# Kernel tuning notes

Hardware: AMD Instinct MI355X
Metric: run time of the kernel (lower is better)

## Reference

```python
import jax, jax.numpy as jnp
import numpy as np

N_HEADS = 16


def setup_inputs() -> dict:
    key = jax.random.key(0)
    ks = jax.random.split(key, 7)
    B, S, E = 4, 2048, 1024
    s = 0.02
    return {
        "x": jax.random.normal(ks[0], (B, S, E), dtype=jnp.float32),
        "Wq": jax.random.normal(ks[1], (E, E), dtype=jnp.float32) * s,
        "bq": jax.random.normal(ks[2], (E,), dtype=jnp.float32) * s,
        "Wk": jax.random.normal(ks[3], (E, E), dtype=jnp.float32) * s,
        "bk": jax.random.normal(ks[4], (E,), dtype=jnp.float32) * s,
        "Wv": jax.random.normal(ks[5], (E, E), dtype=jnp.float32) * s,
        "bv": jax.random.normal(ks[6], (E,), dtype=jnp.float32) * s,
    }


def reference(x, Wq, bq, Wk, bk, Wv, bv):
    B, S, E = x.shape
    H = N_HEADS
    D = E // H  # att_dim
    scale = 1.0 / jnp.sqrt(jnp.asarray(D, dtype=x.dtype))
    # torch Linear: y = x @ W.T + b
    q = (x @ Wq.T + bq).reshape(B, S, H, D)
    k = (x @ Wk.T + bk).reshape(B, S, H, D)
    v = (x @ Wv.T + bv).reshape(B, S, H, D)
    # scores: [B, H, S, S]
    scores = jnp.einsum("bqhd,bkhd->bhqk", q, k) * scale
    attn = jax.nn.softmax(scores, axis=-1)
    out = jnp.einsum("bhqk,bkhd->bqhd", attn, v)
    return out.reshape(B, S, E)
```

## Files before the change

kernel.cpp:

```cpp
#include <hip/hip_runtime.h>
#include <stdint.h>
#include <math.h>

typedef __bf16 bf16;
typedef __attribute__((ext_vector_type(8))) __bf16 bf16x8;
typedef __attribute__((ext_vector_type(4))) __bf16 bf16x4;
typedef __attribute__((ext_vector_type(4))) float f32x4;
typedef unsigned short u16;
typedef unsigned int u32;

#define BATCH 4
#define SEQ   2048
#define EMB   1024
#define HEADS 16
#define HDIM  64
#define BH    (BATCH*HEADS)

#define QSCALE 0.125f

#define OFF_XB 0u
#define OFF_WC 16777216u
#define OFF_Q  23068672u
#define OFF_K  39845888u
#define OFF_VT 56623104u

#define DRAIN_VM asm volatile("s_waitcnt vmcnt(0)" ::: "memory")
#define FENCE_LDS do { \
    asm volatile("s_waitcnt lgkmcnt(0)" ::: "memory"); \
    __builtin_amdgcn_sched_barrier(0); \
} while (0)


__device__ __forceinline__ u16 f2bf(float f) {
    u32 b = __builtin_bit_cast(u32, f);
    return (u16)((b + 0x7fffu + ((b >> 16) & 1u)) >> 16);
}

__global__ void cvt_all(const float* __restrict__ x,
                        const float* __restrict__ wq, const float* __restrict__ wk,
                        const float* __restrict__ wv,
                        u16* __restrict__ xb, u16* __restrict__ wc) {
    const int X4 = (BATCH * SEQ * EMB) / 4;
    const int W4 = (EMB * EMB) / 4;
    const int n4 = X4 + 3 * W4;
    int stride = gridDim.x * blockDim.x;
    for (int i = blockIdx.x * blockDim.x + threadIdx.x; i < n4; i += stride) {
        const float* src; u16* dst; int j;
        if (i < X4)              { src = x;  dst = xb;                j = i; }
        else if (i < X4 + W4)    { src = wq; dst = wc;                j = i - X4; }
        else if (i < X4 + 2*W4)  { src = wk; dst = wc + EMB * EMB;    j = i - X4 - W4; }
        else                     { src = wv; dst = wc + 2 * EMB * EMB; j = i - X4 - 2 * W4; }
        float4 v = reinterpret_cast<const float4*>(src)[j];
        ushort4 o;
        o.x = f2bf(v.x); o.y = f2bf(v.y); o.z = f2bf(v.z); o.w = f2bf(v.w);
        reinterpret_cast<ushort4*>(dst)[j] = o;
    }
}

__global__ __launch_bounds__(256, 3) void qkv_gemm(
    const u16* __restrict__ xb, const u16* __restrict__ wc,
    const float* __restrict__ bq, const float* __restrict__ bk_, const float* __restrict__ bv,
    u16* __restrict__ Qw, u16* __restrict__ Kw, u16* __restrict__ Vt)
{
    __shared__ u16 lds[2 * 128 * 64];
    const int tid = threadIdx.x;
    const int w = tid >> 6, l = tid & 63;
    const int hi = l >> 4, lo = l & 15;
    const int bm = blockIdx.x & 63;
    const int bn = blockIdx.x >> 6;
    const int wm = w >> 1, wn = w & 1;

    const int srow   = l >> 3;
    const int schunk = (l & 7) ^ (srow & 7);

    f32x4 acc[4][4];
#pragma unroll
    for (int i = 0; i < 4; ++i)
#pragma unroll
        for (int j = 0; j < 4; ++j) acc[i][j] = f32x4{0.f, 0.f, 0.f, 0.f};

    for (int t = 0; t < 16; ++t) {
        const u16* asrc = xb + (size_t)(bm * 128 + srow) * 1024 + t * 64 + schunk * 8;
        const u16* bsrc = wc + (size_t)(bn * 128 + srow) * 1024 + t * 64 + schunk * 8;
#pragma unroll
        for (int i = 0; i < 4; ++i) {
            int c = i * 4 + w;
            __builtin_amdgcn_global_load_lds(
                (const __attribute__((address_space(1))) u32*)(asrc + (size_t)c * 8 * 1024),
                (__attribute__((address_space(3))) u32*)(&lds[c * 512]), 16, 0, 0);
            __builtin_amdgcn_global_load_lds(
                (const __attribute__((address_space(1))) u32*)(bsrc + (size_t)c * 8 * 1024),
                (__attribute__((address_space(3))) u32*)(&lds[128 * 64 + c * 512]), 16, 0, 0);
        }
        DRAIN_VM;
        __syncthreads();
#pragma unroll
        for (int kk = 0; kk < 2; ++kk) {
            bf16x8 af[4], bfr[4];
#pragma unroll
            for (int mt = 0; mt < 4; ++mt) {
                int row = wm * 64 + mt * 16 + lo;
                int off = (kk * 64 + hi * 16) ^ ((row & 7) << 4);
                af[mt] = *reinterpret_cast<const bf16x8*>((const char*)lds + row * 128 + off);
            }
#pragma unroll
            for (int nt = 0; nt < 4; ++nt) {
                int row = wn * 64 + nt * 16 + lo;
                int off = (kk * 64 + hi * 16) ^ ((row & 7) << 4);
                bfr[nt] = *reinterpret_cast<const bf16x8*>((const char*)lds + 128 * 64 * 2 + row * 128 + off);
            }
#pragma unroll
            for (int mt = 0; mt < 4; ++mt)
#pragma unroll
                for (int nt = 0; nt < 4; ++nt)
                    acc[mt][nt] = __builtin_amdgcn_mfma_f32_16x16x32_bf16(af[mt], bfr[nt], acc[mt][nt], 0, 0, 0);
        }
        __syncthreads();
    }

#pragma unroll
    for (int nt = 0; nt < 4; ++nt) {
        int ng  = bn * 128 + wn * 64 + nt * 16 + lo;
        int mat = ng >> 10;
        int nl  = ng & 1023;
        int h = nl >> 6, d = nl & 63;
        const float* bp = (mat == 0) ? bq : (mat == 1 ? bk_ : bv);
        float bias = bp[nl];
        float scl = (mat == 0) ? QSCALE : 1.0f;
#pragma unroll
        for (int mt = 0; mt < 4; ++mt) {
            int mbase = bm * 128 + wm * 64 + mt * 16 + hi * 4;
            int b = mbase >> 11, s = mbase & 2047;
            if (mat < 2) {
                u16* dst = (mat == 0) ? Qw : Kw;
                size_t base = ((size_t)(b * 16 + h) * 2048) * 64 + (size_t)d;
#pragma unroll
                for (int r = 0; r < 4; ++r)
                    dst[base + (size_t)(s + r) * 64] = f2bf((acc[mt][nt][r] + bias) * scl);
            } else {
                ushort4 o;
                o.x = f2bf(acc[mt][nt][0] + bias);
                o.y = f2bf(acc[mt][nt][1] + bias);
                o.z = f2bf(acc[mt][nt][2] + bias);
                o.w = f2bf(acc[mt][nt][3] + bias);
                *reinterpret_cast<ushort4*>(&Vt[((size_t)(b * 16 + h) * 64 + d) * 2048 + s]) = o;
            }
        }
    }
}

#define KVB 64
__global__ __launch_bounds__(512, 4) void attn(
    const u16* __restrict__ Qw, const u16* __restrict__ Kw, const u16* __restrict__ Vt,
    float* __restrict__ out)
{
    __shared__ char smem[69632];
    const int tid = threadIdx.x;
    const int w = tid >> 6, l = tid & 63;
    const int hi = l >> 4, lo = l & 15;

    const int bid = blockIdx.x;
    const int xcd = bid & 7, ii = bid >> 3;
    const int bh = xcd * 8 + (ii & 7);
    const int qt = ii >> 3;
    const int bb = bh >> 4, h = bh & 15;
    const int q0w = qt * 256 + w * 32;

    const u16* Qb = Qw + ((size_t)bh * 2048 + q0w) * 64;
    const u16* Kb = Kw + (size_t)bh * 2048 * 64;
    const u16* Vb = Vt + (size_t)bh * 64 * 2048;
    char* bufs = smem;
    char* myP  = smem + 32768 + w * 4608;

    bf16x8 qf[2][2];
#pragma unroll
    for (int qs = 0; qs < 2; ++qs)
#pragma unroll
        for (int kc = 0; kc < 2; ++kc)
            qf[qs][kc] = *reinterpret_cast<const bf16x8*>(Qb + (qs * 16 + lo) * 64 + kc * 32 + hi * 8);

    bf16x8 ones;
#pragma unroll
    for (int i = 0; i < 8; ++i) ones[i] = (__bf16)1.0f;

    const int r0 = w * 8 + (l >> 3);
    const int cs = (l & 7) ^ (r0 & 7);

    const f32x4 zf = {0.f, 0.f, 0.f, 0.f};
    f32x4 acc[4][2];
#pragma unroll
    for (int dt = 0; dt < 4; ++dt)
#pragma unroll
        for (int qs = 0; qs < 2; ++qs) acc[dt][qs] = zf;
    f32x4 den[2] = {zf, zf};

#define STAGE(kvbase, dst)                                                          \
    {                                                                               \
        const u16* srcK = Kb + (size_t)((kvbase) + r0) * 64 + cs * 8;               \
        __builtin_amdgcn_global_load_lds(                                           \
            (const __attribute__((address_space(1))) u32*)srcK,                     \
            (__attribute__((address_space(3))) u32*)((dst) + w * 1024), 16, 0, 0);  \
        const u16* srcV = Vb + (size_t)r0 * 2048 + (kvbase) + cs * 8;               \
        __builtin_amdgcn_global_load_lds(                                           \
            (const __attribute__((address_space(1))) u32*)srcV,                     \
            (__attribute__((address_space(3))) u32*)((dst) + 8192 + w * 1024),      \
            16, 0, 0);                                                              \
    }

    STAGE(0, bufs);
    DRAIN_VM;
    __syncthreads();

    int buf = 0;
    for (int t = 0; t < 2048 / KVB; ++t) {
        if (t + 1 < 2048 / KVB) STAGE((t + 1) * KVB, bufs + (buf ^ 1) * 16384);

        const char* bK = bufs + buf * 16384;
        const char* bV = bK + 8192;

        f32x4 st[4][2];
#pragma unroll
        for (int ct = 0; ct < 4; ++ct) {
            int r = ct * 16 + lo;
            bf16x8 k0 = *reinterpret_cast<const bf16x8*>(bK + r * 128 + ((hi ^ (r & 7)) * 16));
            bf16x8 k1 = *reinterpret_cast<const bf16x8*>(bK + r * 128 + (((4 + hi) ^ (r & 7)) * 16));
#pragma unroll
            for (int qs = 0; qs < 2; ++qs) {
                f32x4 s4 = __builtin_amdgcn_mfma_f32_16x16x32_bf16(k0, qf[qs][0], zf, 0, 0, 0);
                st[ct][qs] = __builtin_amdgcn_mfma_f32_16x16x32_bf16(k1, qf[qs][1], s4, 0, 0, 0);
            }
        }
#pragma unroll
        for (int ct = 0; ct < 4; ++ct)
#pragma unroll
            for (int qs = 0; qs < 2; ++qs) {
                bf16x4 pb;
#pragma unroll
                for (int r = 0; r < 4; ++r) pb[r] = (__bf16)__expf(st[ct][qs][r]);
                *reinterpret_cast<bf16x4*>(myP + (qs * 16 + lo) * 144 + ct * 32 + hi * 8) = pb;
            }
        FENCE_LDS;
#pragma unroll
        for (int hf = 0; hf < 2; ++hf) {
            bf16x8 pf[2];
#pragma unroll
            for (int qs = 0; qs < 2; ++qs)
                pf[qs] = *reinterpret_cast<const bf16x8*>(myP + (qs * 16 + lo) * 144 + hf * 64 + hi * 16);
#pragma unroll
            for (int qs = 0; qs < 2; ++qs)
                den[qs] = __builtin_amdgcn_mfma_f32_16x16x32_bf16(ones, pf[qs], den[qs], 0, 0, 0);
#pragma unroll
            for (int dt = 0; dt < 4; ++dt) {
                int r = dt * 16 + lo;
                bf16x8 vf = *reinterpret_cast<const bf16x8*>(
                    bV + r * 128 + (((hf * 4 + hi) ^ (r & 7)) * 16));
#pragma unroll
                for (int qs = 0; qs < 2; ++qs)
                    acc[dt][qs] = __builtin_amdgcn_mfma_f32_16x16x32_bf16(vf, pf[qs], acc[dt][qs], 0, 0, 0);
            }
        }
        DRAIN_VM;
        __syncthreads();
        buf ^= 1;
    }
#undef STAGE

    float inv[2];
#pragma unroll
    for (int qs = 0; qs < 2; ++qs) inv[qs] = 1.f / den[qs][0];

#pragma unroll
    for (int dt = 0; dt < 4; ++dt)
#pragma unroll
        for (int qs = 0; qs < 2; ++qs) {
            float* og = out + ((size_t)(bb * 2048 + q0w + qs * 16 + lo)) * 1024 + h * 64 + dt * 16 + hi * 4;
            float2 v01 = {acc[dt][qs][0] * inv[qs], acc[dt][qs][1] * inv[qs]};
            float2 v23 = {acc[dt][qs][2] * inv[qs], acc[dt][qs][3] * inv[qs]};
            *reinterpret_cast<float2*>(og)     = v01;
            *reinterpret_cast<float2*>(og + 2) = v23;
        }
}

extern "C" void kernel_launch(void* const* d_in, const int* in_sizes, int n_in,
                              void* d_out, int out_size, void* d_ws, size_t ws_size,
                              hipStream_t stream) {
    (void)in_sizes; (void)n_in; (void)out_size; (void)ws_size;
    const float* x  = (const float*)d_in[0];
    const float* Wq = (const float*)d_in[1];
    const float* bq = (const float*)d_in[2];
    const float* Wk = (const float*)d_in[3];
    const float* bk = (const float*)d_in[4];
    const float* Wv = (const float*)d_in[5];
    const float* bv = (const float*)d_in[6];
    float* out = (float*)d_out;
    char* ws = (char*)d_ws;

    u16* xb = (u16*)(ws + OFF_XB);
    u16* wc = (u16*)(ws + OFF_WC);
    u16* Qw = (u16*)(ws + OFF_Q);
    u16* Kw = (u16*)(ws + OFF_K);
    u16* Vt = (u16*)(ws + OFF_VT);

    cvt_all<<<2048, 256, 0, stream>>>(x, Wq, Wk, Wv, xb, wc);
    qkv_gemm<<<64 * 24, 256, 0, stream>>>(xb, wc, bq, bk, bv, Qw, Kw, Vt);
    attn<<<512, 512, 0, stream>>>(Qw, Kw, Vt, out);
}
```

Baseline: 142.6 us.

## Split each KV tile between wave pairs and reduce partial outputs via LDS

Each pair of waves now shares the same 32 query rows, and each wave handles half of every 64-wide KV tile. Block query coverage drops from 256 to 128 rows, so the grid doubles to 1024 blocks. At the end, partial accumulators and denominators are exchanged through shared memory and summed before normalization. The aim is more parallelism and less serial work per wave, at the cost of twice the K/V staging traffic per query and an extra LDS reduction.

```diff
diff --git a/kernel.cpp b/kernel.cpp
--- a/kernel.cpp
+++ b/kernel.cpp
@@ -158,13 +158,15 @@
     const int tid = threadIdx.x;
     const int w = tid >> 6, l = tid & 63;
     const int hi = l >> 4, lo = l & 15;
+    const int h2 = w & 1;
+    const int qg = w >> 1;
 
     const int bid = blockIdx.x;
     const int xcd = bid & 7, ii = bid >> 3;
     const int bh = xcd * 8 + (ii & 7);
     const int qt = ii >> 3;
     const int bb = bh >> 4, h = bh & 15;
-    const int q0w = qt * 256 + w * 32;
+    const int q0w = qt * 128 + qg * 32;
 
     const u16* Qb = Qw + ((size_t)bh * 2048 + q0w) * 64;
     const u16* Kb = Kw + (size_t)bh * 2048 * 64;
@@ -218,12 +220,12 @@
         const char* bK = bufs + buf * 16384;
         const char* bV = bK + 8192;
 
-        f32x4 st[4][2];
-#pragma unroll
-        for (int ct = 0; ct < 4; ++ct) {
-            int r = ct * 16 + lo;
-            bf16x8 k0 = *reinterpret_cast<const bf16x8*>(bK + r * 128 + ((hi ^ (r & 7)) * 16));
-            bf16x8 k1 = *reinterpret_cast<const bf16x8*>(bK + r * 128 + (((4 + hi) ^ (r & 7)) * 16));
+        f32x4 st[2][2];
+#pragma unroll
+        for (int ct = 0; ct < 2; ++ct) {
+            int r = h2 * 32 + ct * 16 + lo;
+            bf16x8 k0 = *reinterpret_cast<const bf16x8*>(bK + r * 128 + ((hi ^ (lo & 7)) * 16));
+            bf16x8 k1 = *reinterpret_cast<const bf16x8*>(bK + r * 128 + (((4 + hi) ^ (lo & 7)) * 16));
 #pragma unroll
             for (int qs = 0; qs < 2; ++qs) {
                 f32x4 s4 = __builtin_amdgcn_mfma_f32_16x16x32_bf16(k0, qf[qs][0], zf, 0, 0, 0);
@@ -231,7 +233,7 @@
             }
         }
 #pragma unroll
-        for (int ct = 0; ct < 4; ++ct)
+        for (int ct = 0; ct < 2; ++ct)
 #pragma unroll
             for (int qs = 0; qs < 2; ++qs) {
                 bf16x4 pb;
@@ -240,24 +242,21 @@
                 *reinterpret_cast<bf16x4*>(myP + (qs * 16 + lo) * 144 + ct * 32 + hi * 8) = pb;
             }
         FENCE_LDS;
-#pragma unroll
-        for (int hf = 0; hf < 2; ++hf) {
-            bf16x8 pf[2];
+        bf16x8 pf[2];
+#pragma unroll
+        for (int qs = 0; qs < 2; ++qs)
+            pf[qs] = *reinterpret_cast<const bf16x8*>(myP + (qs * 16 + lo) * 144 + hi * 16);
+#pragma unroll
+        for (int qs = 0; qs < 2; ++qs)
+            den[qs] = __builtin_amdgcn_mfma_f32_16x16x32_bf16(ones, pf[qs], den[qs], 0, 0, 0);
+#pragma unroll
+        for (int dt = 0; dt < 4; ++dt) {
+            int r = dt * 16 + lo;
+            bf16x8 vf = *reinterpret_cast<const bf16x8*>(
+                bV + r * 128 + (((h2 * 4 + hi) ^ (lo & 7)) * 16));
 #pragma unroll
             for (int qs = 0; qs < 2; ++qs)
-                pf[qs] = *reinterpret_cast<const bf16x8*>(myP + (qs * 16 + lo) * 144 + hf * 64 + hi * 16);
-#pragma unroll
-            for (int qs = 0; qs < 2; ++qs)
-                den[qs] = __builtin_amdgcn_mfma_f32_16x16x32_bf16(ones, pf[qs], den[qs], 0, 0, 0);
-#pragma unroll
-            for (int dt = 0; dt < 4; ++dt) {
-                int r = dt * 16 + lo;
-                bf16x8 vf = *reinterpret_cast<const bf16x8*>(
-                    bV + r * 128 + (((hf * 4 + hi) ^ (r & 7)) * 16));
-#pragma unroll
-                for (int qs = 0; qs < 2; ++qs)
-                    acc[dt][qs] = __builtin_amdgcn_mfma_f32_16x16x32_bf16(vf, pf[qs], acc[dt][qs], 0, 0, 0);
-            }
+                acc[dt][qs] = __builtin_amdgcn_mfma_f32_16x16x32_bf16(vf, pf[qs], acc[dt][qs], 0, 0, 0);
         }
         DRAIN_VM;
         __syncthreads();
@@ -265,20 +264,39 @@
     }
 #undef STAGE
 
+    float* scr = reinterpret_cast<float*>(smem);
+    float* my = scr + w * 2176 + l * 34;
+#pragma unroll
+    for (int dt = 0; dt < 4; ++dt)
+#pragma unroll
+        for (int qs = 0; qs < 2; ++qs)
+#pragma unroll
+            for (int r = 0; r < 4; ++r)
+                my[dt * 8 + qs * 4 + r] = acc[dt][qs][r];
+    my[32] = den[0][0];
+    my[33] = den[1][0];
+    asm volatile("s_waitcnt lgkmcnt(0)" ::: "memory");
+    __syncthreads();
+    const float* pr = scr + (w ^ 1) * 2176 + l * 34;
     float inv[2];
-#pragma unroll
-    for (int qs = 0; qs < 2; ++qs) inv[qs] = 1.f / den[qs][0];
-
-#pragma unroll
-    for (int dt = 0; dt < 4; ++dt)
+    inv[0] = 1.f / (den[0][0] + pr[32]);
+    inv[1] = 1.f / (den[1][0] + pr[33]);
+
+#pragma unroll
+    for (int dd = 0; dd < 2; ++dd) {
+        int dt = h2 * 2 + dd;
 #pragma unroll
         for (int qs = 0; qs < 2; ++qs) {
+            f32x4 v = acc[dt][qs];
+#pragma unroll
+            for (int r = 0; r < 4; ++r) v[r] += pr[dt * 8 + qs * 4 + r];
             float* og = out + ((size_t)(bb * 2048 + q0w + qs * 16 + lo)) * 1024 + h * 64 + dt * 16 + hi * 4;
-            float2 v01 = {acc[dt][qs][0] * inv[qs], acc[dt][qs][1] * inv[qs]};
-            float2 v23 = {acc[dt][qs][2] * inv[qs], acc[dt][qs][3] * inv[qs]};
+            float2 v01 = {v[0] * inv[qs], v[1] * inv[qs]};
+            float2 v23 = {v[2] * inv[qs], v[3] * inv[qs]};
             *reinterpret_cast<float2*>(og)     = v01;
             *reinterpret_cast<float2*>(og + 2) = v23;
         }
+    }
 }
 
 extern "C" void kernel_launch(void* const* d_in, const int* in_sizes, int n_in,
@@ -303,5 +321,5 @@
 
     cvt_all<<<2048, 256, 0, stream>>>(x, Wq, Wk, Wv, xb, wc);
     qkv_gemm<<<64 * 24, 256, 0, stream>>>(xb, wc, bq, bk, bv, Qw, Kw, Vt);
-    attn<<<512, 512, 0, stream>>>(Qw, Kw, Vt, out);
-}
+    attn<<<1024, 512, 0, stream>>>(Qw, Kw, Vt, out);
+}
```

Result: slower. 161.3 us (+13.1%).
